# Performance work log

Measured on AMD Instinct MI355X. Metric: run time of the kernel, lower is better.

Reference implementation:

```python
import jax, jax.numpy as jnp
import numpy as np

NUM_HEADS = 16
HEAD_DIM = 64  # hidden_size 1024 / 16 heads


def setup_inputs() -> dict:
    key = jax.random.key(0)
    ks = jax.random.split(key, 9)
    B, T, H = 8, 4096, 1024
    s = 1.0 / np.sqrt(H)
    return {
        "hidden_states": jax.random.normal(ks[0], (B, T + 1, H), jnp.float32),
        "cell_state": jax.random.normal(ks[1], (B, H), jnp.float32),
        "Wq": jax.random.normal(ks[2], (H, H), jnp.float32) * s,
        "bq": jax.random.normal(ks[3], (H,), jnp.float32) * 0.02,
        "Wk": jax.random.normal(ks[4], (H, H), jnp.float32) * s,
        "bk": jax.random.normal(ks[5], (H,), jnp.float32) * 0.02,
        "Wv": jax.random.normal(ks[6], (H, H), jnp.float32) * s,
        "bv": jax.random.normal(ks[7], (H,), jnp.float32) * 0.02,
        "attention_mask": jax.random.randint(ks[8], (B, T), 0, 2, jnp.int32),
        "t": T,
    }


def reference(hidden_states, cell_state, Wq, bq, Wk, bk, Wv, bv, attention_mask, t):
    B, _, H = hidden_states.shape
    nh, hd = NUM_HEADS, HEAD_DIM
    # single-query projection: [B, H] -> [B, nh, hd]
    q = (cell_state @ Wq.T + bq).reshape(B, nh, hd)
    # key/value over first t positions: [B, t, H] -> [B, t, nh, hd]
    kv_in = hidden_states[:, :-1]
    k = (kv_in @ Wk.T + bk).reshape(B, t, nh, hd)
    v = (kv_in @ Wv.T + bv).reshape(B, t, nh, hd)
    # GEMV-like scores: [B, nh, t]
    scores = jnp.einsum("bhd,bthd->bht", q, k) / np.sqrt(hd)
    # mask out positions where attention_mask == 0 (intended semantics of
    # inf * eq(mask, 0) in the original, expressed without -inf*0 NaNs)
    mask_add = jnp.where(attention_mask == 0, -jnp.inf, 0.0)[:, None, :]
    probs = jax.nn.softmax(scores + mask_add, axis=-1)
    # dropout is identity in eval mode
    ctx = jnp.einsum("bht,bthd->bhd", probs, v)  # [B, nh, hd]
    return ctx.reshape(B, nh * hd)  # squeeze of [B, 1, H]
```

## Files before the change

kernel.cpp:

```cpp
#include <hip/hip_runtime.h>
#include <math.h>

#define BB 8
#define TT 4096
#define TP1 4097
#define HH 1024
#define NHD 16

__device__ __forceinline__ float dot4(const float4& a, const float4& b) {
  return a.x*b.x + a.y*b.y + a.z*b.z + a.w*b.w;
}

__global__ __launch_bounds__(256) void k_q(const float* __restrict__ cell,
                                           const float* __restrict__ Wq,
                                           const float* __restrict__ bq,
                                           float* __restrict__ qbuf) {
  __shared__ float cs[BB * HH];
  int tid = threadIdx.x;
  #pragma unroll
  for (int m = 0; m < 8; m++) {
    int idx4 = tid + (m << 8);
    ((float4*)cs)[idx4] = ((const float4*)cell)[idx4];
  }
  __syncthreads();
  int jj = tid >> 6, lane = tid & 63;
  int j = blockIdx.x * 4 + jj;
  float acc[BB];
  #pragma unroll
  for (int b = 0; b < BB; b++) acc[b] = 0.f;
  #pragma unroll
  for (int k = 0; k < 4; k++) {
    int i = (k << 8) + (lane << 2);
    float4 w = *(const float4*)&Wq[(size_t)j * HH + i];
    #pragma unroll
    for (int b = 0; b < BB; b++) acc[b] += dot4(w, *(const float4*)&cs[b * HH + i]);
  }
  #pragma unroll
  for (int b = 0; b < BB; b++) {
    acc[b] += __shfl_xor(acc[b], 1);  acc[b] += __shfl_xor(acc[b], 2);
    acc[b] += __shfl_xor(acc[b], 4);  acc[b] += __shfl_xor(acc[b], 8);
    acc[b] += __shfl_xor(acc[b], 16); acc[b] += __shfl_xor(acc[b], 32);
  }
  if (lane == 0) {
    float bqv = bq[j];
    #pragma unroll
    for (int b = 0; b < BB; b++) qbuf[b * HH + j] = 0.125f * (acc[b] + bqv);
  }
}

__global__ __launch_bounds__(256) void k_qwk(const float* __restrict__ qbuf,
                                             const float* __restrict__ Wk,
                                             const float* __restrict__ bk,
                                             float* __restrict__ qWkT,
                                             float* __restrict__ qbk) {
  __shared__ float q_s[BB * 64];
  __shared__ float red[4 * 64 * 9];
  int tid = threadIdx.x;
  int h = blockIdx.x >> 4, ic = blockIdx.x & 15;
  if (tid < 128) {
    int b = tid >> 4, dq = tid & 15;
    ((float4*)q_s)[tid] = ((const float4*)qbuf)[(b << 8) + (h << 4) + dq];
  }
  __syncthreads();
  int dg = tid >> 6, lane = tid & 63;
  int i = (ic << 6) + lane;
  float acc[BB];
  #pragma unroll
  for (int b = 0; b < BB; b++) acc[b] = 0.f;
  #pragma unroll
  for (int dd = 0; dd < 16; dd++) {
    int d = (dg << 4) + dd;
    float wk = Wk[(size_t)((h << 6) + d) * HH + i];
    #pragma unroll
    for (int b = 0; b < BB; b++) acc[b] += q_s[(b << 6) + d] * wk;
  }
  #pragma unroll
  for (int b = 0; b < BB; b++) red[((dg << 6) + lane) * 9 + b] = acc[b];
  __syncthreads();
  #pragma unroll
  for (int r = 0; r < 2; r++) {
    int o = tid + (r << 8);
    int il = o >> 3, b = o & 7;
    float s = 0.f;
    #pragma unroll
    for (int g = 0; g < 4; g++) s += red[((g << 6) + il) * 9 + b];
    qWkT[((size_t)(b << 10) + (ic << 6) + il) * NHD + h] = s;
  }
  if (ic == 0 && tid < 8) {
    float s = 0.f;
    for (int d = 0; d < 64; d++) s += q_s[(tid << 6) + d] * bk[(h << 6) + d];
    qbk[tid * NHD + h] = s;
  }
}

__device__ __forceinline__ void stage_tile(const float* __restrict__ src, float* dst, int tid) {
  #pragma unroll
  for (int m = 0; m < 4; m++) {
    int idx = tid + (m << 8);
    int r = idx >> 4, c4 = idx & 15;
    *(float4*)&dst[r * 68 + (c4 << 2)] = *(const float4*)&src[(size_t)r * HH + (c4 << 2)];
  }
}

__device__ __forceinline__ void compute_chunk(const float* kv_s, const float* __restrict__ qb,
                                              int lane, int w, float* acc) {
  float4 kv[4];
  #pragma unroll
  for (int cq = 0; cq < 4; cq++)
    kv[cq] = *(const float4*)&kv_s[lane * 68 + (w << 4) + (cq << 2)];
  #pragma unroll
  for (int cq = 0; cq < 4; cq++) {
    const float* qp = qb + (cq << 6);
    #pragma unroll
    for (int h = 0; h < NHD; h++)
      acc[h] += kv[cq].x * qp[h] + kv[cq].y * qp[NHD + h] +
                kv[cq].z * qp[2 * NHD + h] + kv[cq].w * qp[3 * NHD + h];
  }
}

__global__ __launch_bounds__(256) void k_scores(const float* __restrict__ hid,
                                                const float* __restrict__ qWkT,
                                                const float* __restrict__ qbk,
                                                const int* __restrict__ mask,
                                                float* __restrict__ probsT,
                                                float* __restrict__ Spart) {
  __shared__ float kv0[64 * 68];
  __shared__ float kv1[64 * 68];
  __shared__ float qbk_s[NHD];
  int tid = threadIdx.x;
  int b = blockIdx.x >> 6, tile = blockIdx.x & 63;
  int t0 = tile << 6;
  if (tid < NHD) qbk_s[tid] = qbk[b * NHD + tid];
  int w = __builtin_amdgcn_readfirstlane(tid >> 6);
  int lane = tid & 63;
  const float* src = hid + ((size_t)(b * TP1) + t0) * HH;
  const float* qB = qWkT + (((size_t)(b << 10) + (w << 4)) << 4);
  float acc[NHD];
  #pragma unroll
  for (int h = 0; h < NHD; h++) acc[h] = 0.f;

  stage_tile(src, kv0, tid);
  __syncthreads();
  for (int cc = 0; cc < 16; cc += 2) {
    stage_tile(src + ((cc + 1) << 6), kv1, tid);
    compute_chunk(kv0, qB + ((cc << 6) << 4), lane, w, acc);
    __syncthreads();
    if (cc + 2 < 16) stage_tile(src + ((cc + 2) << 6), kv0, tid);
    compute_chunk(kv1, qB + (((cc + 1) << 6) << 4), lane, w, acc);
    __syncthreads();
  }

  float* red = kv0;
  float* e_sh = kv1;
  #pragma unroll
  for (int h4 = 0; h4 < 4; h4++)
    *(float4*)&red[((w << 6) + lane) * NHD + (h4 << 2)] =
        make_float4(acc[h4 * 4], acc[h4 * 4 + 1], acc[h4 * 4 + 2], acc[h4 * 4 + 3]);
  __syncthreads();
  int row = tid >> 2, hq = tid & 3;
  float4 s = make_float4(0.f, 0.f, 0.f, 0.f);
  #pragma unroll
  for (int ww = 0; ww < 4; ww++) {
    float4 r = *(const float4*)&red[((ww << 6) + row) * NHD + (hq << 2)];
    s.x += r.x; s.y += r.y; s.z += r.z; s.w += r.w;
  }
  int mk = mask[b * TT + t0 + row];
  float4 e;
  e.x = mk ? __expf(s.x + qbk_s[hq * 4 + 0]) : 0.f;
  e.y = mk ? __expf(s.y + qbk_s[hq * 4 + 1]) : 0.f;
  e.z = mk ? __expf(s.z + qbk_s[hq * 4 + 2]) : 0.f;
  e.w = mk ? __expf(s.w + qbk_s[hq * 4 + 3]) : 0.f;
  *(float4*)&probsT[((size_t)(b * TT + t0 + row)) * NHD + (hq << 2)] = e;
  *(float4*)&e_sh[row * NHD + (hq << 2)] = e;
  __syncthreads();
  if (tid < 64) {
    int g = tid >> 4, h2 = tid & 15;
    float s2 = 0.f;
    #pragma unroll
    for (int j = 0; j < 16; j++) s2 += e_sh[((g + (j << 2)) << 4) + h2];
    s2 += __shfl_xor(s2, 16);
    s2 += __shfl_xor(s2, 32);
    if (tid < 16) Spart[(size_t)((b << 6) + tile) * NHD + h2] = s2;
  }
}

__global__ void k_sinv(const float* __restrict__ Spart, float* __restrict__ Sinv) {
  int tid = threadIdx.x;
  float s = 0.f;
  for (int c = 0; c < 64; c++) s += Spart[(size_t)((tid >> 4) * 64 + c) * NHD + (tid & 15)];
  Sinv[tid] = 1.f / s;
}

__global__ __launch_bounds__(256) void k_ctx(const float* __restrict__ hid,
                                             const float* __restrict__ probsT,
                                             float* __restrict__ ctxin) {
  __shared__ float red2[2][64 * 64];
  int tid = threadIdx.x;
  int b = blockIdx.x >> 6, ic = (blockIdx.x >> 4) & 3, th = blockIdx.x & 15;
  int w = __builtin_amdgcn_readfirstlane(tid >> 6);
  int lane = tid & 63;
  int t0 = (th << 2) + w;
  const float* kvp = hid + (size_t)b * TP1 * HH + (ic << 8) + (lane << 2);
  const float* pb = probsT + ((size_t)(b << 12) + t0) * NHD;
  float4 acc4[NHD];
  #pragma unroll
  for (int h = 0; h < NHD; h++) acc4[h] = make_float4(0.f, 0.f, 0.f, 0.f);
  #pragma unroll 4
  for (int it = 0; it < 64; it++) {
    int t = it << 6;
    float4 kv = *(const float4*)&kvp[(size_t)(t0 + t) * HH];
    const float* pp = pb + (size_t)t * NHD;
    #pragma unroll
    for (int h = 0; h < NHD; h++) {
      float p = pp[h];
      acc4[h].x += kv.x * p; acc4[h].y += kv.y * p;
      acc4[h].z += kv.z * p; acc4[h].w += kv.w * p;
    }
  }
  if (w < 2) {
    #pragma unroll
    for (int h = 0; h < NHD; h++)
      *(float4*)&red2[w][(lane << 6) + (h << 2)] = acc4[h];
  }
  __syncthreads();
  if (w >= 2) {
    #pragma unroll
    for (int h = 0; h < NHD; h++) {
      float4 r = *(const float4*)&red2[w - 2][(lane << 6) + (h << 2)];
      r.x += acc4[h].x; r.y += acc4[h].y; r.z += acc4[h].z; r.w += acc4[h].w;
      *(float4*)&red2[w - 2][(lane << 6) + (h << 2)] = r;
    }
  }
  __syncthreads();
  #pragma unroll
  for (int j = 0; j < 4; j++) {
    int k = tid + (j << 8);
    float4 a = ((const float4*)red2[0])[k];
    float4 c2 = ((const float4*)red2[1])[k];
    int li = k >> 4, h = k & 15;
    float* dst = ctxin + (((size_t)(b << 4) + h) << 10) + (ic << 8) + (li << 2);
    atomicAdd(dst + 0, a.x + c2.x);
    atomicAdd(dst + 1, a.y + c2.y);
    atomicAdd(dst + 2, a.z + c2.z);
    atomicAdd(dst + 3, a.w + c2.w);
  }
}

__global__ __launch_bounds__(256) void k_out(const float* __restrict__ Wv,
                                             const float* __restrict__ bv,
                                             const float* __restrict__ ctxin,
                                             const float* __restrict__ Sinv,
                                             float* __restrict__ out) {
  __shared__ float cs[BB * HH];
  int tid = threadIdx.x;
  int h = blockIdx.x >> 4;
  int j0 = blockIdx.x * 4;
  #pragma unroll
  for (int m = 0; m < 8; m++) {
    int idx4 = tid + (m << 8);
    int b = idx4 >> 8, i4 = idx4 & 255;
    ((float4*)cs)[idx4] = ((const float4*)ctxin)[(((b << 4) + h) << 8) + i4];
  }
  __syncthreads();
  int jj = tid >> 6, lane = tid & 63;
  int j = j0 + jj;
  float acc[BB];
  #pragma unroll
  for (int b = 0; b < BB; b++) acc[b] = 0.f;
  #pragma unroll
  for (int k = 0; k < 4; k++) {
    int i = (k << 8) + (lane << 2);
    float4 w = *(const float4*)&Wv[(size_t)j * HH + i];
    #pragma unroll
    for (int b = 0; b < BB; b++) acc[b] += dot4(w, *(const float4*)&cs[b * HH + i]);
  }
  #pragma unroll
  for (int b = 0; b < BB; b++) {
    acc[b] += __shfl_xor(acc[b], 1);  acc[b] += __shfl_xor(acc[b], 2);
    acc[b] += __shfl_xor(acc[b], 4);  acc[b] += __shfl_xor(acc[b], 8);
    acc[b] += __shfl_xor(acc[b], 16); acc[b] += __shfl_xor(acc[b], 32);
  }
  if (lane == 0) {
    float bvj = bv[j];
    #pragma unroll
    for (int b = 0; b < BB; b++)
      out[b * HH + j] = Sinv[b * NHD + h] * acc[b] + bvj;
  }
}

extern "C" void kernel_launch(void* const* d_in, const int* in_sizes, int n_in,
                              void* d_out, int out_size, void* d_ws, size_t ws_size,
                              hipStream_t stream) {
  const float* hid  = (const float*)d_in[0];
  const float* cell = (const float*)d_in[1];
  const float* Wq   = (const float*)d_in[2];
  const float* bq   = (const float*)d_in[3];
  const float* Wk   = (const float*)d_in[4];
  const float* bk   = (const float*)d_in[5];
  const float* Wv   = (const float*)d_in[6];
  const float* bv   = (const float*)d_in[7];
  const int*  mask  = (const int*)d_in[8];
  float* out = (float*)d_out;

  float* ws = (float*)d_ws;
  float* qbuf    = ws;
  float* qWkT    = ws + 8192;
  float* qbk     = ws + 139264;
  float* probsT  = ws + 139392;
  float* Spart   = ws + 663680;
  float* Sinv    = ws + 671872;
  float* ctxin   = ws + 672000;

  hipMemsetAsync(ctxin, 0, (size_t)BB * NHD * HH * sizeof(float), stream);
  hipLaunchKernelGGL(k_q,      dim3(256), dim3(256), 0, stream, cell, Wq, bq, qbuf);
  hipLaunchKernelGGL(k_qwk,    dim3(256), dim3(256), 0, stream, qbuf, Wk, bk, qWkT, qbk);
  hipLaunchKernelGGL(k_scores, dim3(512), dim3(256), 0, stream, hid, qWkT, qbk, mask, probsT, Spart);
  hipLaunchKernelGGL(k_sinv,   dim3(1),   dim3(128), 0, stream, Spart, Sinv);
  hipLaunchKernelGGL(k_ctx,    dim3(512), dim3(256), 0, stream, hid, probsT, ctxin);
  hipLaunchKernelGGL(k_out,    dim3(256), dim3(256), 0, stream, Wv, bv, ctxin, Sinv, out);
}
```

Before: 296.5 us.

## Retile score kernel with transposed LDS tiles and stage probabilities in LDS for ctx

The score kernel now processes 32-row tiles across twice as many blocks. Each thread computes two rows times 16 heads from a transposed KV tile and a staged qWkT tile, and partial sums are reduced with cross-lane shuffles. The ctx kernel preloads its probability rows into shared memory and batches eight global KV loads per iteration instead of reading probabilities from global memory inside the loop. The aims are more parallelism and memory-level parallelism in both memory-bound passes over hidden_states, at the cost of more LDS traffic, extra transpose stores and higher register pressure.

```diff
diff --git a/kernel.cpp b/kernel.cpp
--- a/kernel.cpp
+++ b/kernel.cpp
@@ -93,128 +93,181 @@
   }
 }
 
-__device__ __forceinline__ void stage_tile(const float* __restrict__ src, float* dst, int tid) {
-  #pragma unroll
-  for (int m = 0; m < 4; m++) {
-    int idx = tid + (m << 8);
-    int r = idx >> 4, c4 = idx & 15;
-    *(float4*)&dst[r * 68 + (c4 << 2)] = *(const float4*)&src[(size_t)r * HH + (c4 << 2)];
-  }
-}
-
-__device__ __forceinline__ void compute_chunk(const float* kv_s, const float* __restrict__ qb,
-                                              int lane, int w, float* acc) {
-  float4 kv[4];
-  #pragma unroll
-  for (int cq = 0; cq < 4; cq++)
-    kv[cq] = *(const float4*)&kv_s[lane * 68 + (w << 4) + (cq << 2)];
-  #pragma unroll
-  for (int cq = 0; cq < 4; cq++) {
-    const float* qp = qb + (cq << 6);
-    #pragma unroll
-    for (int h = 0; h < NHD; h++)
-      acc[h] += kv[cq].x * qp[h] + kv[cq].y * qp[NHD + h] +
-                kv[cq].z * qp[2 * NHD + h] + kv[cq].w * qp[3 * NHD + h];
-  }
-}
-
-__global__ __launch_bounds__(256) void k_scores(const float* __restrict__ hid,
-                                                const float* __restrict__ qWkT,
-                                                const float* __restrict__ qbk,
-                                                const int* __restrict__ mask,
-                                                float* __restrict__ probsT,
-                                                float* __restrict__ Spart) {
-  __shared__ float kv0[64 * 68];
-  __shared__ float kv1[64 * 68];
+__global__ __launch_bounds__(256, 4) void k_scores(const float* __restrict__ hid,
+                                                   const float* __restrict__ qWkT,
+                                                   const float* __restrict__ qbk,
+                                                   const int* __restrict__ mask,
+                                                   float* __restrict__ probsT,
+                                                   float* __restrict__ Spart) {
+  __shared__ float S[6912];
   __shared__ float qbk_s[NHD];
   int tid = threadIdx.x;
-  int b = blockIdx.x >> 6, tile = blockIdx.x & 63;
-  int t0 = tile << 6;
+  int b = blockIdx.x >> 7, tile = blockIdx.x & 127;
+  int t0 = tile << 5;
   if (tid < NHD) qbk_s[tid] = qbk[b * NHD + tid];
-  int w = __builtin_amdgcn_readfirstlane(tid >> 6);
-  int lane = tid & 63;
+  int kq = tid >> 4, rg = tid & 15;
+  int r = tid >> 4, c4 = tid & 15;
   const float* src = hid + ((size_t)(b * TP1) + t0) * HH;
-  const float* qB = qWkT + (((size_t)(b << 10) + (w << 4)) << 4);
-  float acc[NHD];
-  #pragma unroll
-  for (int h = 0; h < NHD; h++) acc[h] = 0.f;
-
-  stage_tile(src, kv0, tid);
-  __syncthreads();
-  for (int cc = 0; cc < 16; cc += 2) {
-    stage_tile(src + ((cc + 1) << 6), kv1, tid);
-    compute_chunk(kv0, qB + ((cc << 6) << 4), lane, w, acc);
+  const float4* qsrc4 = (const float4*)qWkT;
+
+  float* KV0 = S;
+  float* KV1 = S + 2176;
+  float* QT0 = S + 4352;
+  float* QT1 = S + 5632;
+
+  {
+    float4 v0 = *(const float4*)&src[(size_t)r * HH + (c4 << 2)];
+    float4 v1 = *(const float4*)&src[(size_t)(r + 16) * HH + (c4 << 2)];
+    float4 vq = qsrc4[(b << 12) + tid];
+    #pragma unroll
+    for (int c = 0; c < 4; c++) {
+      KV0[((c4 << 2) + c) * 34 + r]      = (&v0.x)[c];
+      KV0[((c4 << 2) + c) * 34 + r + 16] = (&v1.x)[c];
+    }
+    *(float4*)&QT0[(tid >> 2) * 20 + ((tid & 3) << 2)] = vq;
+  }
+  __syncthreads();
+
+  float acc0[16], acc1[16];
+  #pragma unroll
+  for (int h = 0; h < 16; h++) { acc0[h] = 0.f; acc1[h] = 0.f; }
+
+  for (int cc = 0; cc < 16; cc++) {
+    int cur = cc & 1;
+    const float* kvb = cur ? KV1 : KV0;
+    const float* qtb = cur ? QT1 : QT0;
+    float* dkv = cur ? KV0 : KV1;
+    float* dqt = cur ? QT0 : QT1;
+    float4 v0, v1, vq;
+    bool hasNext = (cc < 15);
+    if (hasNext) {
+      const float* s2 = src + ((cc + 1) << 6);
+      v0 = *(const float4*)&s2[(size_t)r * HH + (c4 << 2)];
+      v1 = *(const float4*)&s2[(size_t)(r + 16) * HH + (c4 << 2)];
+      vq = qsrc4[(b << 12) + ((cc + 1) << 8) + tid];
+    }
+    #pragma unroll
+    for (int ii = 0; ii < 4; ii++) {
+      int il = (kq << 2) + ii;
+      float2 kv2 = *(const float2*)&kvb[il * 34 + (rg << 1)];
+      float qv[16];
+      *(float4*)&qv[0]  = *(const float4*)&qtb[il * 20];
+      *(float4*)&qv[4]  = *(const float4*)&qtb[il * 20 + 4];
+      *(float4*)&qv[8]  = *(const float4*)&qtb[il * 20 + 8];
+      *(float4*)&qv[12] = *(const float4*)&qtb[il * 20 + 12];
+      #pragma unroll
+      for (int h = 0; h < 16; h++) {
+        acc0[h] += kv2.x * qv[h];
+        acc1[h] += kv2.y * qv[h];
+      }
+    }
+    if (hasNext) {
+      #pragma unroll
+      for (int c = 0; c < 4; c++) {
+        dkv[((c4 << 2) + c) * 34 + r]      = (&v0.x)[c];
+        dkv[((c4 << 2) + c) * 34 + r + 16] = (&v1.x)[c];
+      }
+      *(float4*)&dqt[(tid >> 2) * 20 + ((tid & 3) << 2)] = vq;
+    }
     __syncthreads();
-    if (cc + 2 < 16) stage_tile(src + ((cc + 2) << 6), kv0, tid);
-    compute_chunk(kv1, qB + (((cc + 1) << 6) << 4), lane, w, acc);
-    __syncthreads();
-  }
-
-  float* red = kv0;
-  float* e_sh = kv1;
-  #pragma unroll
-  for (int h4 = 0; h4 < 4; h4++)
-    *(float4*)&red[((w << 6) + lane) * NHD + (h4 << 2)] =
-        make_float4(acc[h4 * 4], acc[h4 * 4 + 1], acc[h4 * 4 + 2], acc[h4 * 4 + 3]);
-  __syncthreads();
-  int row = tid >> 2, hq = tid & 3;
-  float4 s = make_float4(0.f, 0.f, 0.f, 0.f);
-  #pragma unroll
-  for (int ww = 0; ww < 4; ww++) {
-    float4 r = *(const float4*)&red[((ww << 6) + row) * NHD + (hq << 2)];
-    s.x += r.x; s.y += r.y; s.z += r.z; s.w += r.w;
-  }
-  int mk = mask[b * TT + t0 + row];
-  float4 e;
-  e.x = mk ? __expf(s.x + qbk_s[hq * 4 + 0]) : 0.f;
-  e.y = mk ? __expf(s.y + qbk_s[hq * 4 + 1]) : 0.f;
-  e.z = mk ? __expf(s.z + qbk_s[hq * 4 + 2]) : 0.f;
-  e.w = mk ? __expf(s.w + qbk_s[hq * 4 + 3]) : 0.f;
-  *(float4*)&probsT[((size_t)(b * TT + t0 + row)) * NHD + (hq << 2)] = e;
-  *(float4*)&e_sh[row * NHD + (hq << 2)] = e;
+  }
+
+  #pragma unroll
+  for (int h = 0; h < 16; h++) {
+    acc0[h] += __shfl_xor(acc0[h], 16); acc0[h] += __shfl_xor(acc0[h], 32);
+    acc1[h] += __shfl_xor(acc1[h], 16); acc1[h] += __shfl_xor(acc1[h], 32);
+  }
+  int w = tid >> 6;
+  if ((tid & 48) == 0) {
+    float* rp = &S[((w << 4) + rg) * 36];
+    *(float4*)&rp[0]  = make_float4(acc0[0],  acc0[1],  acc0[2],  acc0[3]);
+    *(float4*)&rp[4]  = make_float4(acc0[4],  acc0[5],  acc0[6],  acc0[7]);
+    *(float4*)&rp[8]  = make_float4(acc0[8],  acc0[9],  acc0[10], acc0[11]);
+    *(float4*)&rp[12] = make_float4(acc0[12], acc0[13], acc0[14], acc0[15]);
+    *(float4*)&rp[16] = make_float4(acc1[0],  acc1[1],  acc1[2],  acc1[3]);
+    *(float4*)&rp[20] = make_float4(acc1[4],  acc1[5],  acc1[6],  acc1[7]);
+    *(float4*)&rp[24] = make_float4(acc1[8],  acc1[9],  acc1[10], acc1[11]);
+    *(float4*)&rp[28] = make_float4(acc1[12], acc1[13], acc1[14], acc1[15]);
+  }
+  __syncthreads();
+  if (tid < 128) {
+    int row = tid >> 2, hq = tid & 3;
+    float4 sv = make_float4(0.f, 0.f, 0.f, 0.f);
+    #pragma unroll
+    for (int ww = 0; ww < 4; ww++) {
+      const float* rp = &S[((ww << 4) + (row >> 1)) * 36 + ((row & 1) << 4) + (hq << 2)];
+      float4 rv = *(const float4*)rp;
+      sv.x += rv.x; sv.y += rv.y; sv.z += rv.z; sv.w += rv.w;
+    }
+    int mk = mask[b * TT + t0 + row];
+    float4 e;
+    e.x = mk ? __expf(sv.x + qbk_s[(hq << 2) + 0]) : 0.f;
+    e.y = mk ? __expf(sv.y + qbk_s[(hq << 2) + 1]) : 0.f;
+    e.z = mk ? __expf(sv.z + qbk_s[(hq << 2) + 2]) : 0.f;
+    e.w = mk ? __expf(sv.w + qbk_s[(hq << 2) + 3]) : 0.f;
+    *(float4*)&probsT[((size_t)(b * TT + t0 + row)) * NHD + (hq << 2)] = e;
+    *(float4*)&S[4352 + (row << 4) + (hq << 2)] = e;
+  }
   __syncthreads();
   if (tid < 64) {
     int g = tid >> 4, h2 = tid & 15;
     float s2 = 0.f;
     #pragma unroll
-    for (int j = 0; j < 16; j++) s2 += e_sh[((g + (j << 2)) << 4) + h2];
+    for (int j = 0; j < 8; j++) s2 += S[4352 + ((g + (j << 2)) << 4) + h2];
     s2 += __shfl_xor(s2, 16);
     s2 += __shfl_xor(s2, 32);
-    if (tid < 16) Spart[(size_t)((b << 6) + tile) * NHD + h2] = s2;
+    if (tid < 16) Spart[((size_t)(b << 7) + tile) * NHD + h2] = s2;
   }
 }
 
 __global__ void k_sinv(const float* __restrict__ Spart, float* __restrict__ Sinv) {
   int tid = threadIdx.x;
   float s = 0.f;
-  for (int c = 0; c < 64; c++) s += Spart[(size_t)((tid >> 4) * 64 + c) * NHD + (tid & 15)];
+  for (int c = 0; c < 128; c++) s += Spart[(size_t)((tid >> 4) * 128 + c) * NHD + (tid & 15)];
   Sinv[tid] = 1.f / s;
 }
 
 __global__ __launch_bounds__(256) void k_ctx(const float* __restrict__ hid,
                                              const float* __restrict__ probsT,
                                              float* __restrict__ ctxin) {
+  __shared__ float p_s[256 * 16];
   __shared__ float red2[2][64 * 64];
   int tid = threadIdx.x;
   int b = blockIdx.x >> 6, ic = (blockIdx.x >> 4) & 3, th = blockIdx.x & 15;
   int w = __builtin_amdgcn_readfirstlane(tid >> 6);
   int lane = tid & 63;
+  #pragma unroll
+  for (int m = 0; m < 4; m++) {
+    int idx = tid + (m << 8);
+    int rr = idx >> 2, qq = idx & 3;
+    int wp = rr >> 6, k = rr & 63;
+    ((float4*)p_s)[idx] =
+        *(const float4*)&probsT[((size_t)(b << 12) + (th << 2) + wp + (k << 6)) * NHD + (qq << 2)];
+  }
+  __syncthreads();
   int t0 = (th << 2) + w;
   const float* kvp = hid + (size_t)b * TP1 * HH + (ic << 8) + (lane << 2);
-  const float* pb = probsT + ((size_t)(b << 12) + t0) * NHD;
   float4 acc4[NHD];
   #pragma unroll
   for (int h = 0; h < NHD; h++) acc4[h] = make_float4(0.f, 0.f, 0.f, 0.f);
-  #pragma unroll 4
-  for (int it = 0; it < 64; it++) {
-    int t = it << 6;
-    float4 kv = *(const float4*)&kvp[(size_t)(t0 + t) * HH];
-    const float* pp = pb + (size_t)t * NHD;
-    #pragma unroll
-    for (int h = 0; h < NHD; h++) {
-      float p = pp[h];
-      acc4[h].x += kv.x * p; acc4[h].y += kv.y * p;
-      acc4[h].z += kv.z * p; acc4[h].w += kv.w * p;
+  for (int it8 = 0; it8 < 64; it8 += 8) {
+    float4 kv[8];
+    #pragma unroll
+    for (int m = 0; m < 8; m++)
+      kv[m] = *(const float4*)&kvp[(size_t)(t0 + ((it8 + m) << 6)) * HH];
+    #pragma unroll
+    for (int m = 0; m < 8; m++) {
+      const float* pp = &p_s[((w << 6) + it8 + m) << 4];
+      float pv[16];
+      *(float4*)&pv[0]  = *(const float4*)&pp[0];
+      *(float4*)&pv[4]  = *(const float4*)&pp[4];
+      *(float4*)&pv[8]  = *(const float4*)&pp[8];
+      *(float4*)&pv[12] = *(const float4*)&pp[12];
+      #pragma unroll
+      for (int h = 0; h < NHD; h++) {
+        acc4[h].x += kv[m].x * pv[h]; acc4[h].y += kv[m].y * pv[h];
+        acc4[h].z += kv[m].z * pv[h]; acc4[h].w += kv[m].w * pv[h];
+      }
     }
   }
   if (w < 2) {
@@ -308,14 +361,14 @@
   float* qbk     = ws + 139264;
   float* probsT  = ws + 139392;
   float* Spart   = ws + 663680;
-  float* Sinv    = ws + 671872;
-  float* ctxin   = ws + 672000;
+  float* Sinv    = ws + 680064;
+  float* ctxin   = ws + 680192;
 
   hipMemsetAsync(ctxin, 0, (size_t)BB * NHD * HH * sizeof(float), stream);
-  hipLaunchKernelGGL(k_q,      dim3(256), dim3(256), 0, stream, cell, Wq, bq, qbuf);
-  hipLaunchKernelGGL(k_qwk,    dim3(256), dim3(256), 0, stream, qbuf, Wk, bk, qWkT, qbk);
-  hipLaunchKernelGGL(k_scores, dim3(512), dim3(256), 0, stream, hid, qWkT, qbk, mask, probsT, Spart);
-  hipLaunchKernelGGL(k_sinv,   dim3(1),   dim3(128), 0, stream, Spart, Sinv);
-  hipLaunchKernelGGL(k_ctx,    dim3(512), dim3(256), 0, stream, hid, probsT, ctxin);
-  hipLaunchKernelGGL(k_out,    dim3(256), dim3(256), 0, stream, Wv, bv, ctxin, Sinv, out);
-}
+  hipLaunchKernelGGL(k_q,      dim3(256),  dim3(256), 0, stream, cell, Wq, bq, qbuf);
+  hipLaunchKernelGGL(k_qwk,    dim3(256),  dim3(256), 0, stream, qbuf, Wk, bk, qWkT, qbk);
+  hipLaunchKernelGGL(k_scores, dim3(1024), dim3(256), 0, stream, hid, qWkT, qbk, mask, probsT, Spart);
+  hipLaunchKernelGGL(k_sinv,   dim3(1),    dim3(128), 0, stream, Spart, Sinv);
+  hipLaunchKernelGGL(k_ctx,    dim3(512),  dim3(256), 0, stream, hid, probsT, ctxin);
+  hipLaunchKernelGGL(k_out,    dim3(256),  dim3(256), 0, stream, Wv, bv, ctxin, Sinv, out);
+}
```

New measurement: 289.6 us. 2.3% less time.

## Fuse score and context passes to read hidden states once per tile

Applied to the files above, without the earlier changes.

Merges the score kernel and the probability-weighted context kernel into one kernel. Each block stages a 16-row slice of hidden states in LDS (XOR-swizzled), computes the exponentiated scores, and immediately accumulates exp-weighted rows into per-head context partials. This removes the second full read of the 128MB hidden-state tensor, the probsT round trip and the atomicAdd reduction. Per-block partials are then summed by a new reduce kernel instead. The cost is a larger partial buffer (about 32MB write plus read), heavy LDS use (~134KB, one block per CU) and higher register pressure.

```diff
diff --git a/kernel.cpp b/kernel.cpp
--- a/kernel.cpp
+++ b/kernel.cpp
@@ -93,157 +93,183 @@
   }
 }
 
-__device__ __forceinline__ void stage_tile(const float* __restrict__ src, float* dst, int tid) {
-  #pragma unroll
-  for (int m = 0; m < 4; m++) {
+#define QT_OFF   0
+#define KV_OFF   16384
+#define E_OFF    32768
+#define RED_OFF  33024
+#define RED2_OFF 34048
+#define QBK_OFF  34112
+#define MSK_OFF  34128
+
+__global__ __launch_bounds__(256, 1) void k_sctx(const float* __restrict__ hid,
+                                                 const float* __restrict__ qWkT,
+                                                 const float* __restrict__ qbk,
+                                                 const int* __restrict__ mask,
+                                                 float* __restrict__ ctxp,
+                                                 float* __restrict__ Spart) {
+  __shared__ float S[34192];
+  int tid = threadIdx.x;
+  int b = blockIdx.x >> 6, g = blockIdx.x & 63;
+  int t0 = g << 6;
+  int kq = tid >> 4, rg4 = tid & 15;
+  int kqm = kq & 3;
+
+  #pragma unroll
+  for (int m = 0; m < 16; m++) {
     int idx = tid + (m << 8);
-    int r = idx >> 4, c4 = idx & 15;
-    *(float4*)&dst[r * 68 + (c4 << 2)] = *(const float4*)&src[(size_t)r * HH + (c4 << 2)];
-  }
-}
-
-__device__ __forceinline__ void compute_chunk(const float* kv_s, const float* __restrict__ qb,
-                                              int lane, int w, float* acc) {
-  float4 kv[4];
-  #pragma unroll
-  for (int cq = 0; cq < 4; cq++)
-    kv[cq] = *(const float4*)&kv_s[lane * 68 + (w << 4) + (cq << 2)];
-  #pragma unroll
-  for (int cq = 0; cq < 4; cq++) {
-    const float* qp = qb + (cq << 6);
-    #pragma unroll
-    for (int h = 0; h < NHD; h++)
-      acc[h] += kv[cq].x * qp[h] + kv[cq].y * qp[NHD + h] +
-                kv[cq].z * qp[2 * NHD + h] + kv[cq].w * qp[3 * NHD + h];
-  }
-}
-
-__global__ __launch_bounds__(256) void k_scores(const float* __restrict__ hid,
-                                                const float* __restrict__ qWkT,
-                                                const float* __restrict__ qbk,
-                                                const int* __restrict__ mask,
-                                                float* __restrict__ probsT,
-                                                float* __restrict__ Spart) {
-  __shared__ float kv0[64 * 68];
-  __shared__ float kv1[64 * 68];
-  __shared__ float qbk_s[NHD];
-  int tid = threadIdx.x;
-  int b = blockIdx.x >> 6, tile = blockIdx.x & 63;
-  int t0 = tile << 6;
-  if (tid < NHD) qbk_s[tid] = qbk[b * NHD + tid];
-  int w = __builtin_amdgcn_readfirstlane(tid >> 6);
-  int lane = tid & 63;
-  const float* src = hid + ((size_t)(b * TP1) + t0) * HH;
-  const float* qB = qWkT + (((size_t)(b << 10) + (w << 4)) << 4);
-  float acc[NHD];
-  #pragma unroll
-  for (int h = 0; h < NHD; h++) acc[h] = 0.f;
-
-  stage_tile(src, kv0, tid);
-  __syncthreads();
-  for (int cc = 0; cc < 16; cc += 2) {
-    stage_tile(src + ((cc + 1) << 6), kv1, tid);
-    compute_chunk(kv0, qB + ((cc << 6) << 4), lane, w, acc);
+    float4 v = ((const float4*)qWkT)[((size_t)b << 12) + idx];
+    *(float4*)&S[QT_OFF + (idx << 2)] = v;
+  }
+  if (tid < NHD) S[QBK_OFF + tid] = qbk[b * NHD + tid];
+  if (tid < 64) S[MSK_OFF + tid] = (float)mask[b * TT + t0 + tid];
+
+  const float* src = hid + ((size_t)b * TP1 + t0) * HH;
+  float4 stg[16];
+  #pragma unroll
+  for (int m = 0; m < 16; m++)
+    stg[m] = *(const float4*)&src[(size_t)m * HH + (tid << 2)];
+
+  float4 acc4[16];
+  #pragma unroll
+  for (int h = 0; h < 16; h++) acc4[h] = make_float4(0.f, 0.f, 0.f, 0.f);
+  float sp = 0.f;
+
+  #pragma unroll 1
+  for (int tt = 0; tt < 4; tt++) {
+    #pragma unroll
+    for (int m = 0; m < 16; m++)
+      *(float4*)&S[KV_OFF + (((m << 8) + (tid ^ m)) << 2)] = stg[m];
     __syncthreads();
-    if (cc + 2 < 16) stage_tile(src + ((cc + 2) << 6), kv0, tid);
-    compute_chunk(kv1, qB + (((cc + 1) << 6) << 4), lane, w, acc);
+
+    float accs[16];
+    #pragma unroll
+    for (int k = 0; k < 16; k++) accs[k] = 0.f;
+    #pragma unroll
+    for (int qq = 0; qq < 16; qq++) {
+      int q = (kq << 4) + qq;
+      float4 kvq = *(const float4*)&S[KV_OFF + (((rg4 << 8) + (q ^ rg4)) << 2)];
+      #pragma unroll
+      for (int c = 0; c < 4; c++) {
+        float kvv = (&kvq.x)[c];
+        int i16 = ((q << 2) + c) << 4;
+        #pragma unroll
+        for (int j = 0; j < 4; j++) {
+          int s = j ^ kqm;
+          float4 qv = *(const float4*)&S[QT_OFF + i16 + (s << 2)];
+          accs[(j << 2) + 0] += kvv * qv.x;
+          accs[(j << 2) + 1] += kvv * qv.y;
+          accs[(j << 2) + 2] += kvv * qv.z;
+          accs[(j << 2) + 3] += kvv * qv.w;
+        }
+      }
+    }
+    {
+      float tmp[16];
+      #pragma unroll
+      for (int j = 0; j < 4; j++)
+        #pragma unroll
+        for (int c = 0; c < 4; c++)
+          tmp[(j << 2) + c] = __shfl_xor(accs[((j ^ 1) << 2) + c], 16);
+      #pragma unroll
+      for (int k = 0; k < 16; k++) accs[k] += tmp[k];
+      #pragma unroll
+      for (int j = 0; j < 4; j++)
+        #pragma unroll
+        for (int c = 0; c < 4; c++)
+          tmp[(j << 2) + c] = __shfl_xor(accs[((j ^ 2) << 2) + c], 32);
+      #pragma unroll
+      for (int k = 0; k < 16; k++) accs[k] += tmp[k];
+    }
+    if ((tid & 48) == 0) {
+      int w = tid >> 6;
+      #pragma unroll
+      for (int j = 0; j < 4; j++)
+        *(float4*)&S[RED_OFF + (w << 8) + (rg4 << 4) + (j << 2)] =
+            make_float4(accs[(j << 2)], accs[(j << 2) + 1],
+                        accs[(j << 2) + 2], accs[(j << 2) + 3]);
+    }
     __syncthreads();
-  }
-
-  float* red = kv0;
-  float* e_sh = kv1;
-  #pragma unroll
-  for (int h4 = 0; h4 < 4; h4++)
-    *(float4*)&red[((w << 6) + lane) * NHD + (h4 << 2)] =
-        make_float4(acc[h4 * 4], acc[h4 * 4 + 1], acc[h4 * 4 + 2], acc[h4 * 4 + 3]);
-  __syncthreads();
-  int row = tid >> 2, hq = tid & 3;
+
+    {
+      int rge = tid >> 4, he = tid & 15;
+      float sv = S[RED_OFF + (rge << 4) + he] + S[RED_OFF + 256 + (rge << 4) + he] +
+                 S[RED_OFF + 512 + (rge << 4) + he] + S[RED_OFF + 768 + (rge << 4) + he];
+      sv += S[QBK_OFF + he];
+      float mkf = S[MSK_OFF + (tt << 4) + rge];
+      float ev = (mkf != 0.f) ? __expf(sv) : 0.f;
+      S[E_OFF + (rge << 4) + he] = ev;
+      sp += ev;
+    }
+    __syncthreads();
+
+    if (tt < 3) {
+      const float* s2 = src + ((size_t)((tt + 1) << 4)) * HH;
+      #pragma unroll
+      for (int m = 0; m < 16; m++)
+        stg[m] = *(const float4*)&s2[(size_t)m * HH + (tid << 2)];
+    }
+
+    #pragma unroll
+    for (int r = 0; r < 16; r++) {
+      float4 kvq = *(const float4*)&S[KV_OFF + (((r << 8) + (tid ^ r)) << 2)];
+      float4 e0 = *(const float4*)&S[E_OFF + (r << 4)];
+      float4 e1 = *(const float4*)&S[E_OFF + (r << 4) + 4];
+      float4 e2 = *(const float4*)&S[E_OFF + (r << 4) + 8];
+      float4 e3 = *(const float4*)&S[E_OFF + (r << 4) + 12];
+      #define PVH(hh, ev) \
+        acc4[hh].x += kvq.x * (ev); acc4[hh].y += kvq.y * (ev); \
+        acc4[hh].z += kvq.z * (ev); acc4[hh].w += kvq.w * (ev);
+      PVH(0, e0.x)  PVH(1, e0.y)  PVH(2, e0.z)  PVH(3, e0.w)
+      PVH(4, e1.x)  PVH(5, e1.y)  PVH(6, e1.z)  PVH(7, e1.w)
+      PVH(8, e2.x)  PVH(9, e2.y)  PVH(10, e2.z) PVH(11, e2.w)
+      PVH(12, e3.x) PVH(13, e3.y) PVH(14, e3.z) PVH(15, e3.w)
+      #undef PVH
+    }
+    __syncthreads();
+  }
+
+  {
+    float* cp = ctxp + ((((size_t)b * 64 + g) * 16) << 10) + (tid << 2);
+    #pragma unroll
+    for (int h = 0; h < 16; h++)
+      *(float4*)&cp[(size_t)h << 10] = acc4[h];
+  }
+
+  {
+    sp += __shfl_xor(sp, 16);
+    sp += __shfl_xor(sp, 32);
+    int w = tid >> 6;
+    if ((tid & 48) == 0) S[RED2_OFF + (w << 4) + (tid & 15)] = sp;
+  }
+  __syncthreads();
+  if (tid < 16) {
+    float s = S[RED2_OFF + tid] + S[RED2_OFF + 16 + tid] +
+              S[RED2_OFF + 32 + tid] + S[RED2_OFF + 48 + tid];
+    Spart[(((size_t)b << 6) + g) * NHD + tid] = s;
+  }
+}
+
+__global__ void k_sinv(const float* __restrict__ Spart, float* __restrict__ Sinv) {
+  int tid = threadIdx.x;
+  int b = tid >> 4, h = tid & 15;
+  float s = 0.f;
+  #pragma unroll 8
+  for (int c = 0; c < 64; c++) s += Spart[(size_t)((b << 6) + c) * NHD + h];
+  Sinv[tid] = 1.f / s;
+}
+
+__global__ __launch_bounds__(256) void k_reduce(const float* __restrict__ ctxp,
+                                                float* __restrict__ ctxin) {
+  int tid = threadIdx.x;
+  int b = blockIdx.x >> 4, h = blockIdx.x & 15;
+  const float4* cp4 = (const float4*)ctxp;
   float4 s = make_float4(0.f, 0.f, 0.f, 0.f);
-  #pragma unroll
-  for (int ww = 0; ww < 4; ww++) {
-    float4 r = *(const float4*)&red[((ww << 6) + row) * NHD + (hq << 2)];
-    s.x += r.x; s.y += r.y; s.z += r.z; s.w += r.w;
-  }
-  int mk = mask[b * TT + t0 + row];
-  float4 e;
-  e.x = mk ? __expf(s.x + qbk_s[hq * 4 + 0]) : 0.f;
-  e.y = mk ? __expf(s.y + qbk_s[hq * 4 + 1]) : 0.f;
-  e.z = mk ? __expf(s.z + qbk_s[hq * 4 + 2]) : 0.f;
-  e.w = mk ? __expf(s.w + qbk_s[hq * 4 + 3]) : 0.f;
-  *(float4*)&probsT[((size_t)(b * TT + t0 + row)) * NHD + (hq << 2)] = e;
-  *(float4*)&e_sh[row * NHD + (hq << 2)] = e;
-  __syncthreads();
-  if (tid < 64) {
-    int g = tid >> 4, h2 = tid & 15;
-    float s2 = 0.f;
-    #pragma unroll
-    for (int j = 0; j < 16; j++) s2 += e_sh[((g + (j << 2)) << 4) + h2];
-    s2 += __shfl_xor(s2, 16);
-    s2 += __shfl_xor(s2, 32);
-    if (tid < 16) Spart[(size_t)((b << 6) + tile) * NHD + h2] = s2;
-  }
-}
-
-__global__ void k_sinv(const float* __restrict__ Spart, float* __restrict__ Sinv) {
-  int tid = threadIdx.x;
-  float s = 0.f;
-  for (int c = 0; c < 64; c++) s += Spart[(size_t)((tid >> 4) * 64 + c) * NHD + (tid & 15)];
-  Sinv[tid] = 1.f / s;
-}
-
-__global__ __launch_bounds__(256) void k_ctx(const float* __restrict__ hid,
-                                             const float* __restrict__ probsT,
-                                             float* __restrict__ ctxin) {
-  __shared__ float red2[2][64 * 64];
-  int tid = threadIdx.x;
-  int b = blockIdx.x >> 6, ic = (blockIdx.x >> 4) & 3, th = blockIdx.x & 15;
-  int w = __builtin_amdgcn_readfirstlane(tid >> 6);
-  int lane = tid & 63;
-  int t0 = (th << 2) + w;
-  const float* kvp = hid + (size_t)b * TP1 * HH + (ic << 8) + (lane << 2);
-  const float* pb = probsT + ((size_t)(b << 12) + t0) * NHD;
-  float4 acc4[NHD];
-  #pragma unroll
-  for (int h = 0; h < NHD; h++) acc4[h] = make_float4(0.f, 0.f, 0.f, 0.f);
-  #pragma unroll 4
-  for (int it = 0; it < 64; it++) {
-    int t = it << 6;
-    float4 kv = *(const float4*)&kvp[(size_t)(t0 + t) * HH];
-    const float* pp = pb + (size_t)t * NHD;
-    #pragma unroll
-    for (int h = 0; h < NHD; h++) {
-      float p = pp[h];
-      acc4[h].x += kv.x * p; acc4[h].y += kv.y * p;
-      acc4[h].z += kv.z * p; acc4[h].w += kv.w * p;
-    }
-  }
-  if (w < 2) {
-    #pragma unroll
-    for (int h = 0; h < NHD; h++)
-      *(float4*)&red2[w][(lane << 6) + (h << 2)] = acc4[h];
-  }
-  __syncthreads();
-  if (w >= 2) {
-    #pragma unroll
-    for (int h = 0; h < NHD; h++) {
-      float4 r = *(const float4*)&red2[w - 2][(lane << 6) + (h << 2)];
-      r.x += acc4[h].x; r.y += acc4[h].y; r.z += acc4[h].z; r.w += acc4[h].w;
-      *(float4*)&red2[w - 2][(lane << 6) + (h << 2)] = r;
-    }
-  }
-  __syncthreads();
-  #pragma unroll
-  for (int j = 0; j < 4; j++) {
-    int k = tid + (j << 8);
-    float4 a = ((const float4*)red2[0])[k];
-    float4 c2 = ((const float4*)red2[1])[k];
-    int li = k >> 4, h = k & 15;
-    float* dst = ctxin + (((size_t)(b << 4) + h) << 10) + (ic << 8) + (li << 2);
-    atomicAdd(dst + 0, a.x + c2.x);
-    atomicAdd(dst + 1, a.y + c2.y);
-    atomicAdd(dst + 2, a.z + c2.z);
-    atomicAdd(dst + 3, a.w + c2.w);
-  }
+  #pragma unroll 8
+  for (int g = 0; g < 64; g++) {
+    float4 v = cp4[((((size_t)b * 64 + g) * 16 + h) << 8) + tid];
+    s.x += v.x; s.y += v.y; s.z += v.z; s.w += v.w;
+  }
+  ((float4*)ctxin)[(((size_t)(b << 4) + h) << 8) + tid] = s;
 }
 
 __global__ __launch_bounds__(256) void k_out(const float* __restrict__ Wv,
@@ -306,16 +332,15 @@
   float* qbuf    = ws;
   float* qWkT    = ws + 8192;
   float* qbk     = ws + 139264;
-  float* probsT  = ws + 139392;
-  float* Spart   = ws + 663680;
-  float* Sinv    = ws + 671872;
-  float* ctxin   = ws + 672000;
-
-  hipMemsetAsync(ctxin, 0, (size_t)BB * NHD * HH * sizeof(float), stream);
+  float* Spart   = ws + 139392;
+  float* Sinv    = ws + 147584;
+  float* ctxin   = ws + 147712;
+  float* ctxp    = ws + 278784;
+
   hipLaunchKernelGGL(k_q,      dim3(256), dim3(256), 0, stream, cell, Wq, bq, qbuf);
   hipLaunchKernelGGL(k_qwk,    dim3(256), dim3(256), 0, stream, qbuf, Wk, bk, qWkT, qbk);
-  hipLaunchKernelGGL(k_scores, dim3(512), dim3(256), 0, stream, hid, qWkT, qbk, mask, probsT, Spart);
+  hipLaunchKernelGGL(k_sctx,   dim3(512), dim3(256), 0, stream, hid, qWkT, qbk, mask, ctxp, Spart);
   hipLaunchKernelGGL(k_sinv,   dim3(1),   dim3(128), 0, stream, Spart, Sinv);
-  hipLaunchKernelGGL(k_ctx,    dim3(512), dim3(256), 0, stream, hid, probsT, ctxin);
+  hipLaunchKernelGGL(k_reduce, dim3(128), dim3(256), 0, stream, ctxp, ctxin);
   hipLaunchKernelGGL(k_out,    dim3(256), dim3(256), 0, stream, Wv, bv, ctxin, Sinv, out);
 }
```

Measured after the change: 307.5 us. 3.7% more time.
